# Kernel optimization log

Measured on AMD Instinct MI355X. Metric: run time of the kernel, lower is better.

Reference implementation:

```python
import jax, jax.numpy as jnp
import numpy as np

GRID_SIZE, SPLINE_ORDER = 5, 3
NUM_BASES = GRID_SIZE + SPLINE_ORDER  # 8
GRID = jnp.asarray(np.arange(-SPLINE_ORDER, GRID_SIZE + SPLINE_ORDER + 1, dtype=np.float32) * (2.0 / GRID_SIZE) - 1.0)  # (12,)


def _b_splines(x):
    # x: (M, F) -> (M, F, NUM_BASES), Cox-de Boor recursion on shared uniform grid
    g = GRID
    xe = x[..., None]
    b = ((xe >= g[:-1]) & (xe < g[1:])).astype(x.dtype)
    for k in range(1, SPLINE_ORDER + 1):
        b = ((xe - g[:-(k + 1)]) / (g[k:-1] - g[:-(k + 1)]) * b[..., :-1]
             + (g[k + 1:] - xe) / (g[k + 1:] - g[1:-k]) * b[..., 1:])
    return b


def _kan_linear(x, base_w, spline_w):
    # x: (M, Fin); base_w: (Fout, Fin); spline_w: (Fout, Fin, NUM_BASES)
    base = jax.nn.silu(x) @ base_w.T
    spl = _b_splines(x).reshape(x.shape[0], -1) @ spline_w.reshape(spline_w.shape[0], -1).T
    return base + spl


def _ln(x, g, b, eps=1e-5):
    mu = jnp.mean(x, -1, keepdims=True)
    var = jnp.var(x, -1, keepdims=True)
    return (x - mu) * jax.lax.rsqrt(var + eps) * g + b


def _dwconv(img, w, b):
    C = img.shape[1]
    out = jax.lax.conv_general_dilated(img, w, (1, 1), 'SAME',
        dimension_numbers=('NCHW', 'OIHW', 'NCHW'), feature_group_count=C)
    return out + b[None, :, None, None]


def _dw_bn_relu(x, H, W, w, b, gamma, beta, eps=1e-5):
    # BN in eval mode with running_mean=0, running_var=1
    B, N, C = x.shape
    img = x.transpose(0, 2, 1).reshape(B, C, H, W)
    out = _dwconv(img, w, b)
    out = out * (gamma * (1.0 / np.sqrt(1.0 + eps)))[None, :, None, None] + beta[None, :, None, None]
    out = jax.nn.relu(out)
    return out.reshape(B, C, H * W).transpose(0, 2, 1)


def _cross_selective_scan(img, x_proj_w, dt_w, dt_b, A_logs, Ds, g, b):
    # img: (B, Di, H, W). 4-direction diagonal/antidiagonal selective scan (VMamba-style).
    B, Di, H, W = img.shape
    L = H * W
    K = x_proj_w.shape[0]
    R = dt_w.shape[2]
    Nst = A_logs.shape[1]
    i = jnp.arange(H)[:, None]
    j = jnp.arange(W)[None, :]
    diag = (i + j) % W
    adiag = (j - i) % W
    diag_inv = (jnp.arange(W)[None, :] - i) % W
    adiag_inv = (jnp.arange(W)[None, :] + i) % W

    def gather(x, idx):
        gth = jnp.take_along_axis(x, idx[None, None], axis=3)  # (B,Di,H,W)
        return gth.transpose(0, 1, 3, 2).reshape(B, Di, L)

    def scatter(flat, idx_inv):
        v = flat.reshape(B, Di, W, H).transpose(0, 1, 3, 2)
        return jnp.take_along_axis(v, idx_inv[None, None], axis=3)

    gd, gad = gather(img, diag), gather(img, adiag)
    xs = jnp.stack([gd, gad, jnp.flip(gd, -1), jnp.flip(gad, -1)], axis=1)  # (B,K,Di,L)
    x_dbl = jnp.einsum('bkdl,kcd->bkcl', xs, x_proj_w)
    dts, Bs, Cs = jnp.split(x_dbl, [R, R + Nst], axis=2)  # (B,K,R,L),(B,K,N,L),(B,K,N,L)
    dts = jnp.einsum('bkrl,kdr->bkdl', dts, dt_w)
    delta = jax.nn.softplus(dts + dt_b[None, :, :, None])  # (B,K,Di,L)
    A = -jnp.exp(A_logs).reshape(K, Di, Nst)

    def step(hst, inp):
        u_t, d_t, B_t, C_t = inp  # (B,K,Di),(B,K,Di),(B,K,N),(B,K,N)
        dA = jnp.exp(d_t[..., None] * A)
        hst = dA * hst + (d_t * u_t)[..., None] * B_t[:, :, None, :]
        return hst, jnp.einsum('bkdn,bkn->bkd', hst, C_t)

    h0 = jnp.zeros((B, K, Di, Nst), img.dtype)
    _, ys = jax.lax.scan(step, h0,
        (xs.transpose(3, 0, 1, 2), delta.transpose(3, 0, 1, 2),
         Bs.transpose(3, 0, 1, 2), Cs.transpose(3, 0, 1, 2)))  # ys: (L,B,K,Di)
    ys = ys.transpose(1, 2, 3, 0) + Ds.reshape(K, Di)[None, :, :, None] * xs  # (B,K,Di,L)
    yd = ys[:, 0] + jnp.flip(ys[:, 2], -1)
    ya = ys[:, 1] + jnp.flip(ys[:, 3], -1)
    y = scatter(yd, diag_inv) + scatter(ya, adiag_inv)  # (B,Di,H,W)
    y = y.reshape(B, Di, L).transpose(0, 2, 1)
    return _ln(y, g, b)  # (B,L,Di)


def setup_inputs():
    key = jax.random.key(0)
    ks = iter(jax.random.split(key, 48))
    B, H, W, C = 4, 64, 64, 96
    Di, K, Nst = 2 * C, 4, 16
    R = int(np.ceil(C / 16))
    L = H * W

    def rn(shape, s=0.05):
        return jax.random.normal(next(ks), shape, jnp.float32) * s

    return dict(
        x=jax.random.normal(next(ks), (B, L, C), jnp.float32),
        H=H, W=W,
        norm1_g=jnp.ones((C,), jnp.float32), norm1_b=jnp.zeros((C,), jnp.float32),
        in_proj_w=rn((2 * Di, C)),
        conv_w=rn((Di, 1, 3, 3), 0.2), conv_b=jnp.zeros((Di,), jnp.float32),
        x_proj_w=rn((K, R + 2 * Nst, Di)),
        dt_w=rn((K, Di, R), 0.1), dt_b=rn((K, Di), 0.1),
        A_logs=jax.random.uniform(next(ks), (K * Di, Nst), jnp.float32),
        Ds=jnp.ones((K * Di,), jnp.float32),
        out_norm_g=jnp.ones((Di,), jnp.float32), out_norm_b=jnp.zeros((Di,), jnp.float32),
        out_proj_w=rn((C, Di)),
        norm2_g=jnp.ones((C,), jnp.float32), norm2_b=jnp.zeros((C,), jnp.float32),
        fc1_base_w=rn((C, C)), fc1_spline_w=rn((C, C, NUM_BASES), 0.02),
        fc2_base_w=rn((C, C)), fc2_spline_w=rn((C, C, NUM_BASES), 0.02),
        fc3_base_w=rn((C, C)), fc3_spline_w=rn((C, C, NUM_BASES), 0.02),
        dw1_w=rn((C, 1, 3, 3), 0.2), dw1_b=jnp.zeros((C,), jnp.float32),
        dw1_g=jnp.ones((C,), jnp.float32), dw1_beta=jnp.zeros((C,), jnp.float32),
        dw2_w=rn((C, 1, 3, 3), 0.2), dw2_b=jnp.zeros((C,), jnp.float32),
        dw2_g=jnp.ones((C,), jnp.float32), dw2_beta=jnp.zeros((C,), jnp.float32),
        dw3_w=rn((C, 1, 3, 3), 0.2), dw3_b=jnp.zeros((C,), jnp.float32),
        dw3_g=jnp.ones((C,), jnp.float32), dw3_beta=jnp.zeros((C,), jnp.float32),
    )


def reference(x, H, W, norm1_g, norm1_b, in_proj_w, conv_w, conv_b, x_proj_w,
              dt_w, dt_b, A_logs, Ds, out_norm_g, out_norm_b, out_proj_w,
              norm2_g, norm2_b, fc1_base_w, fc1_spline_w, fc2_base_w, fc2_spline_w,
              fc3_base_w, fc3_spline_w, dw1_w, dw1_b, dw1_g, dw1_beta,
              dw2_w, dw2_b, dw2_g, dw2_beta, dw3_w, dw3_b, dw3_g, dw3_beta):
    B, L, C = x.shape
    # --- SS2D branch ---
    h = _ln(x, norm1_g, norm1_b)
    xz = h @ in_proj_w.T  # (B,L,2*Di)
    Di = xz.shape[-1] // 2
    xin, z = xz[..., :Di], xz[..., Di:]
    img = xin.transpose(0, 2, 1).reshape(B, Di, H, W)
    img = jax.nn.silu(_dwconv(img, conv_w, conv_b))
    y = _cross_selective_scan(img, x_proj_w, dt_w, dt_b, A_logs, Ds, out_norm_g, out_norm_b)
    y = y * jax.nn.silu(z)
    x = x + y @ out_proj_w.T
    # --- KAN branch ---
    h = _ln(x, norm2_g, norm2_b)
    M = B * L
    t = _kan_linear(h.reshape(M, C), fc1_base_w, fc1_spline_w).reshape(B, L, -1)
    t = _dw_bn_relu(t, H, W, dw1_w, dw1_b, dw1_g, dw1_beta)
    t = _kan_linear(t.reshape(M, -1), fc2_base_w, fc2_spline_w).reshape(B, L, -1)
    t = _dw_bn_relu(t, H, W, dw2_w, dw2_b, dw2_g, dw2_beta)
    t = _kan_linear(t.reshape(M, -1), fc3_base_w, fc3_spline_w).reshape(B, L, -1)
    t = _dw_bn_relu(t, H, W, dw3_w, dw3_b, dw3_g, dw3_beta)
    return x + t
```

## Files before the change

kernel.cpp:

```cpp
#include <hip/hip_runtime.h>
#include <math.h>

constexpr int B_  = 4;
constexpr int H_  = 64;
constexpr int W_  = 64;
constexpr int C_  = 96;
constexpr int L_  = H_ * W_;
constexpr int DI  = 192;
constexpr int K_  = 4;
constexpr int NST = 16;
constexpr int R_  = 6;
constexpr int M_  = B_ * L_;

constexpr int NCH = 128;
constexpr int CL  = 32;
constexpr int DG  = 12;

constexpr int KANK = 864;
constexpr int KLAY = 96 * KANK;

typedef __attribute__((ext_vector_type(8))) short short8;
typedef __attribute__((ext_vector_type(4))) float floatx4;
typedef __attribute__((ext_vector_type(4))) unsigned short ushort4v;

__device__ __forceinline__ float wave_sum64(float v) {
#pragma unroll
  for (int off = 1; off < 64; off <<= 1) v += __shfl_xor(v, off, 64);
  return v;
}

__device__ __forceinline__ float exp2_hw(float x) {
  return __builtin_amdgcn_exp2f(x);
}

__device__ __forceinline__ int pos_kl(int k, int l) {
  int ll = (k >= 2) ? (L_ - 1 - l) : l;
  int i = ll & 63;
  int j = ll >> 6;
  int col = ((k & 1) == 0) ? ((i + j) & 63) : ((j - i) & 63);
  return (i << 6) + col;
}

__device__ __forceinline__ int pos_pair(int pr, int ll) {
  int i = ll & 63, j = ll >> 6;
  int col = (pr == 0) ? ((i + j) & 63) : ((j - i) & 63);
  return (i << 6) + col;
}

__device__ __forceinline__ float silu_f(float x) {
  return x / (1.f + __expf(-x));
}

__device__ __forceinline__ float softplus_fast(float s) {
  return fmaxf(s, 0.f) + __logf(1.f + __expf(-fabsf(s)));
}

__device__ __forceinline__ unsigned short f2bf(float f) {
  unsigned u = __float_as_uint(f);
  unsigned r = (u + 0x7FFFu + ((u >> 16) & 1u)) >> 16;
  return (unsigned short)r;
}

__device__ __forceinline__ float bf2f(unsigned short h) {
  return __uint_as_float(((unsigned)h) << 16);
}

__device__ __forceinline__ void spline8(float x, float* bb ) {
#pragma unroll
  for (int i2 = 0; i2 < 11; i2++) {
    float g0 = 0.4f * i2 - 2.2f;
    float g1 = 0.4f * i2 - 1.8f;
    bb[i2] = (x >= g0 && x < g1) ? 1.f : 0.f;
  }
#pragma unroll
  for (int k2 = 1; k2 <= 3; k2++) {
    float invd = 1.f / (0.4f * k2);
#pragma unroll
    for (int i2 = 0; i2 + k2 < 11; i2++) {
      float gi   = 0.4f * i2 - 2.2f;
      float gik1 = 0.4f * (i2 + k2 + 1) - 2.2f;
      bb[i2] = (x - gi) * invd * bb[i2] + (gik1 - x) * invd * bb[i2 + 1];
    }
  }
}

__global__ __launch_bounds__(256) void ln96_kernel(const float* __restrict__ in,
    const float* __restrict__ g, const float* __restrict__ b,
    float* __restrict__ out) {
  int wave = blockIdx.x * 4 + (threadIdx.x >> 6);
  int lane = threadIdx.x & 63;
  const float* rp = in + (size_t)wave * C_;
  float v0 = rp[lane];
  float v1 = (lane < C_ - 64) ? rp[lane + 64] : 0.f;
  float s  = wave_sum64(v0 + v1);
  float s2 = wave_sum64(v0 * v0 + v1 * v1);
  float mean = s * (1.f / C_);
  float var  = s2 * (1.f / C_) - mean * mean;
  float inv  = rsqrtf(var + 1e-5f);
  float* op = out + (size_t)wave * C_;
  op[lane] = (v0 - mean) * inv * g[lane] + b[lane];
  if (lane < C_ - 64) op[lane + 64] = (v1 - mean) * inv * g[lane + 64] + b[lane + 64];
}

__global__ __launch_bounds__(256) void prep_inproj_kernel(const float* __restrict__ w,
    unsigned short* __restrict__ wio) {
  int idx = blockIdx.x * 256 + threadIdx.x;
  if (idx >= 384 * 96) return;
  float v = w[idx];
  unsigned short hh = f2bf(v);
  wio[idx] = hh;
  wio[36864 + idx] = f2bf(v - bf2f(hh));
}

__global__ __launch_bounds__(256) void gemm_in_mfma_kernel(const float* __restrict__ h,
    const unsigned short* __restrict__ wio, float* __restrict__ xin,
    float* __restrict__ z) {
  __shared__ __align__(16) unsigned short Wh[96][104];
  __shared__ __align__(16) unsigned short Wl[96][104];
  int row0 = blockIdx.x * 64;
  int tid = threadIdx.x;
  int wv = tid >> 6, lane = tid & 63, mrow = lane & 15, quad = lane >> 4;

  short8 ah[3], al[3];
  const float* hr = h + (size_t)(row0 + wv * 16 + mrow) * C_;
#pragma unroll
  for (int ks = 0; ks < 3; ks++) {
    float4 va = *(const float4*)&hr[ks * 32 + quad * 8];
    float4 vb = *(const float4*)&hr[ks * 32 + quad * 8 + 4];
    float f[8] = {va.x, va.y, va.z, va.w, vb.x, vb.y, vb.z, vb.w};
    short8 hh, ll;
#pragma unroll
    for (int q = 0; q < 8; q++) {
      unsigned short hv = f2bf(f[q]);
      hh[q] = (short)hv;
      ll[q] = (short)f2bf(f[q] - bf2f(hv));
    }
    ah[ks] = hh; al[ks] = ll;
  }
  for (int nc = 0; nc < 4; nc++) {
    if (nc) __syncthreads();
    for (int t = tid; t < 96 * 12; t += 256) {
      int j = t / 12, u = t % 12;
      *(short8*)&Wh[j][u * 8] = *(const short8*)&wio[(size_t)(nc * 96 + j) * 96 + u * 8];
      *(short8*)&Wl[j][u * 8] = *(const short8*)&wio[(size_t)(384 + nc * 96 + j) * 96 + u * 8];
    }
    __syncthreads();
    floatx4 acc[6];
#pragma unroll
    for (int q = 0; q < 6; q++) acc[q] = (floatx4)(0.f);
#pragma unroll
    for (int ks = 0; ks < 3; ks++) {
#pragma unroll
      for (int nt = 0; nt < 6; nt++) {
        short8 bh = *(const short8*)&Wh[nt * 16 + mrow][ks * 32 + quad * 8];
        short8 bl = *(const short8*)&Wl[nt * 16 + mrow][ks * 32 + quad * 8];
        acc[nt] = __builtin_amdgcn_mfma_f32_16x16x32_bf16(ah[ks], bh, acc[nt], 0, 0, 0);
        acc[nt] = __builtin_amdgcn_mfma_f32_16x16x32_bf16(al[ks], bh, acc[nt], 0, 0, 0);
        acc[nt] = __builtin_amdgcn_mfma_f32_16x16x32_bf16(ah[ks], bl, acc[nt], 0, 0, 0);
      }
    }
#pragma unroll
    for (int nt = 0; nt < 6; nt++) {
      int j = nc * 96 + nt * 16 + mrow;
#pragma unroll
      for (int rg = 0; rg < 4; rg++) {
        int row = row0 + wv * 16 + quad * 4 + rg;
        float v = acc[nt][rg];
        if (j < DI) xin[(size_t)row * DI + j] = v;
        else        z[(size_t)row * DI + (j - DI)] = v;
      }
    }
  }
}

__global__ __launch_bounds__(192) void conv_silu_kernel(const float* __restrict__ xin,
    const float* __restrict__ cw, const float* __restrict__ cb, float* __restrict__ imgT) {
  int p = blockIdx.x;
  int b = p >> 12;
  int ij = p & 4095;
  int i = ij >> 6, j = ij & 63;
  int c = threadIdx.x;
  float acc = cb[c];
#pragma unroll
  for (int di = -1; di <= 1; di++) {
    int ii = i + di;
    if (ii < 0 || ii >= H_) continue;
#pragma unroll
    for (int dj = -1; dj <= 1; dj++) {
      int jj = j + dj;
      if (jj < 0 || jj >= W_) continue;
      acc += xin[((size_t)b * L_ + ii * W_ + jj) * DI + c] * cw[c * 9 + (di + 1) * 3 + (dj + 1)];
    }
  }
  imgT[(size_t)p * DI + c] = silu_f(acc);
}

__global__ __launch_bounds__(256) void xdbl_mfma_kernel(const float* __restrict__ imgT,
    const float* __restrict__ xpw, float* __restrict__ dts_g,
    float* __restrict__ BsT, float* __restrict__ CsT) {
  __shared__ __align__(16) unsigned short Ah[64][104];
  __shared__ __align__(16) unsigned short Al[64][104];
  __shared__ __align__(16) unsigned short Wh[48][104];
  __shared__ __align__(16) unsigned short Wl[48][104];
  __shared__ int pos_s[64];

  int blk = blockIdx.x;
  int lt = blk & 63;
  int bk = blk >> 6;
  int k = bk % K_, b = bk / K_;
  int l0 = lt * 64;
  int tid = threadIdx.x;
  int wid = tid >> 6;
  int lane = tid & 63;
  int mrow = lane & 15, quad = lane >> 4;

  if (tid < 64) pos_s[tid] = pos_kl(k, l0 + tid);
  __syncthreads();

  floatx4 acc[3];
#pragma unroll
  for (int q = 0; q < 3; q++) acc[q] = (floatx4)(0.f);

  const float* img_b = imgT + (size_t)b * L_ * DI;

  for (int kc = 0; kc < 2; kc++) {
    if (kc) __syncthreads();
    for (int t = tid; t < 64 * 24; t += 256) {
      int li = t / 24, c4 = (t % 24) * 4;
      const float4 v = *(const float4*)&img_b[(size_t)pos_s[li] * DI + kc * 96 + c4];
      ushort4v h4, l4;
      float fv[4] = {v.x, v.y, v.z, v.w};
#pragma unroll
      for (int q = 0; q < 4; q++) {
        unsigned short hh = f2bf(fv[q]);
        h4[q] = hh;
        l4[q] = f2bf(fv[q] - bf2f(hh));
      }
      *(ushort4v*)&Ah[li][c4] = h4;
      *(ushort4v*)&Al[li][c4] = l4;
    }
    for (int t = tid; t < 48 * 24; t += 256) {
      int j = t / 24, c4 = (t % 24) * 4;
      ushort4v h4 = (ushort4v)0, l4 = (ushort4v)0;
      if (j < 38) {
        int c = (j < 32) ? (j + 6) : (j - 32);
        const float4 v = *(const float4*)&xpw[((size_t)(k * 38 + c)) * DI + kc * 96 + c4];
        float fv[4] = {v.x, v.y, v.z, v.w};
#pragma unroll
        for (int q = 0; q < 4; q++) {
          unsigned short hh = f2bf(fv[q]);
          h4[q] = hh;
          l4[q] = f2bf(fv[q] - bf2f(hh));
        }
      }
      *(ushort4v*)&Wh[j][c4] = h4;
      *(ushort4v*)&Wl[j][c4] = l4;
    }
    __syncthreads();
#pragma unroll
    for (int ks = 0; ks < 3; ks++) {
      short8 ah = *(const short8*)&Ah[wid * 16 + mrow][ks * 32 + quad * 8];
      short8 al = *(const short8*)&Al[wid * 16 + mrow][ks * 32 + quad * 8];
#pragma unroll
      for (int nt = 0; nt < 3; nt++) {
        short8 bh = *(const short8*)&Wh[nt * 16 + mrow][ks * 32 + quad * 8];
        short8 bl = *(const short8*)&Wl[nt * 16 + mrow][ks * 32 + quad * 8];
        acc[nt] = __builtin_amdgcn_mfma_f32_16x16x32_bf16(ah, bh, acc[nt], 0, 0, 0);
        acc[nt] = __builtin_amdgcn_mfma_f32_16x16x32_bf16(al, bh, acc[nt], 0, 0, 0);
        acc[nt] = __builtin_amdgcn_mfma_f32_16x16x32_bf16(ah, bl, acc[nt], 0, 0, 0);
      }
    }
  }
  size_t bkL = (size_t)(b * K_ + k) * L_ + l0;
#pragma unroll
  for (int rg = 0; rg < 4; rg++) {
    int grow = wid * 16 + quad * 4 + rg;
    size_t base = (bkL + grow) * NST;
    BsT[base + mrow] = acc[0][rg];
    CsT[base + mrow] = acc[1][rg];
    if (mrow < R_) dts_g[(bkL + grow) * 8 + mrow] = acc[2][rg];
  }
}

__global__ __launch_bounds__(192) void scan1_kernel(const float* __restrict__ imgT,
    const float* __restrict__ dts_g, const float* __restrict__ BsT,
    const float* __restrict__ A_logs, const float* __restrict__ dtw,
    const float* __restrict__ dtb, float* __restrict__ hend,
    float* __restrict__ aprod) {
  __shared__ float bs_s[CL][NST];
  __shared__ float dt_s[CL][8];
  int blk = blockIdx.x;
  int c = blk % NCH;
  int tmp = blk / NCH;
  int k = tmp % K_, b = tmp / K_;
  int l0 = c * CL;
  int d = threadIdx.x;
  const float* img_b = imgT + (size_t)b * L_ * DI;
  {
    const float* Bs_bk = BsT + ((size_t)(b * K_ + k) * L_ + l0) * NST;
    for (int t = d; t < CL * NST; t += 192) bs_s[t >> 4][t & 15] = Bs_bk[t];
    const float* Dt = dts_g + ((size_t)(b * K_ + k) * L_ + l0) * 8;
    for (int t = d; t < CL * 8; t += 192) dt_s[t >> 3][t & 7] = Dt[t];
  }
  float A2[NST];
  {
    const float* ap = A_logs + (size_t)(k * DI + d) * NST;
#pragma unroll
    for (int n = 0; n < NST; n++) A2[n] = -__expf(ap[n]) * 1.44269504f;
  }
  float w6[6], bias;
  {
    const float* wp = dtw + ((size_t)k * DI + d) * R_;
#pragma unroll
    for (int r = 0; r < 6; r++) w6[r] = wp[r];
    bias = dtb[k * DI + d];
  }
  __syncthreads();
  float h[NST];
#pragma unroll
  for (int n = 0; n < NST; n++) h[n] = 0.f;
  float sum_dlt = 0.f;
  float u = img_b[(size_t)pos_kl(k, l0) * DI + d];
  for (int l = 0; l < CL; l++) {
    float uc = u;
    if (l + 1 < CL) u = img_b[(size_t)pos_kl(k, l0 + l + 1) * DI + d];
    const float* dv = dt_s[l];
    float s = bias + w6[0] * dv[0] + w6[1] * dv[1] + w6[2] * dv[2]
                   + w6[3] * dv[3] + w6[4] * dv[4] + w6[5] * dv[5];
    float dc = softplus_fast(s);
    sum_dlt += dc;
    float du = dc * uc;
#pragma unroll
    for (int n = 0; n < NST; n++) {
      float dA = exp2_hw(dc * A2[n]);
      h[n] = dA * h[n] + du * bs_s[l][n];
    }
  }
  size_t base = ((size_t)(b * K_ + k) * NCH + c) * (DI * NST) + d;
#pragma unroll
  for (int n = 0; n < NST; n++) {
    hend[base + (size_t)n * DI]  = h[n];
    aprod[base + (size_t)n * DI] = exp2_hw(A2[n] * sum_dlt);
  }
}

__global__ __launch_bounds__(256) void scan_carry_kernel(float* __restrict__ hend,
    const float* __restrict__ aprod) {
  constexpr int PF = 8;
  int blk = blockIdx.x;
  int part = blk % DG;
  int bk = blk / DG;
  const size_t DNS = (size_t)DI * NST;
  size_t base = (size_t)bk * NCH * DNS + (size_t)part * 256 + threadIdx.x;
  float hb[PF], ab[PF];
#pragma unroll
  for (int q = 0; q < PF; q++) {
    hb[q] = hend[base + (size_t)q * DNS];
    ab[q] = aprod[base + (size_t)q * DNS];
  }
  float carry = 0.f;
  for (int c0 = 0; c0 < NCH; c0 += PF) {
    float hn[PF], an[PF];
    if (c0 + PF < NCH) {
#pragma unroll
      for (int q = 0; q < PF; q++) {
        hn[q] = hend[base + (size_t)(c0 + PF + q) * DNS];
        an[q] = aprod[base + (size_t)(c0 + PF + q) * DNS];
      }
    } else {
#pragma unroll
      for (int q = 0; q < PF; q++) { hn[q] = 0.f; an[q] = 0.f; }
    }
#pragma unroll
    for (int q = 0; q < PF; q++) {
      hend[base + (size_t)(c0 + q) * DNS] = carry;
      carry = ab[q] * carry + hb[q];
    }
#pragma unroll
    for (int q = 0; q < PF; q++) { hb[q] = hn[q]; ab[q] = an[q]; }
  }
}

__global__ __launch_bounds__(192) void scan2_pair_kernel(const float* __restrict__ imgT,
    const float* __restrict__ dts_g, const float* __restrict__ BsT,
    const float* __restrict__ CsT, const float* __restrict__ A_logs,
    const float* __restrict__ dtw, const float* __restrict__ dtb,
    const float* __restrict__ Ds, const float* __restrict__ carry_in,
    float* __restrict__ y02, float* __restrict__ y13) {
  __shared__ float bsf[CL][NST], csf[CL][NST], bsr[CL][NST], csr[CL][NST];
  __shared__ float dtf[CL][8], dtr[CL][8];
  __shared__ float y_lds[CL][DI];
  int blk = blockIdx.x;
  int c  = blk % NCH;
  int pr = (blk / NCH) & 1;
  int b  = blk / (2 * NCH);
  int kf = pr, kr = pr + 2;
  int p0 = c * CL;
  int d = threadIdx.x;
  const float* img_b = imgT + (size_t)b * L_ * DI;
  {
    const float* Bf = BsT + ((size_t)(b * K_ + kf) * L_ + p0) * NST;
    const float* Cf = CsT + ((size_t)(b * K_ + kf) * L_ + p0) * NST;
    for (int t = d; t < CL * NST; t += 192) {
      bsf[t >> 4][t & 15] = Bf[t];
      csf[t >> 4][t & 15] = Cf[t];
    }
    const float* Br = BsT + (size_t)(b * K_ + kr) * L_ * NST;
    const float* Cr = CsT + (size_t)(b * K_ + kr) * L_ * NST;
    for (int t = d; t < CL * NST; t += 192) {
      int q = t >> 4, n = t & 15;
      size_t sr = (size_t)(L_ - 1 - p0 - q) * NST + n;
      bsr[q][n] = Br[sr];
      csr[q][n] = Cr[sr];
    }
    const float* Df = dts_g + ((size_t)(b * K_ + kf) * L_ + p0) * 8;
    for (int t = d; t < CL * 8; t += 192) dtf[t >> 3][t & 7] = Df[t];
    const float* Dr = dts_g + (size_t)(b * K_ + kr) * L_ * 8;
    for (int t = d; t < CL * 8; t += 192) {
      int q = t >> 3, r = t & 7;
      dtr[q][r] = Dr[(size_t)(L_ - 1 - p0 - q) * 8 + r];
    }
  }
  __syncthreads();
  float A2[NST], h[NST], w6[6], bias;
  {
    const float* ap = A_logs + (size_t)(kf * DI + d) * NST;
#pragma unroll
    for (int n = 0; n < NST; n++) A2[n] = -__expf(ap[n]) * 1.44269504f;
    size_t cb = ((size_t)(b * K_ + kf) * NCH + c) * (DI * NST) + d;
#pragma unroll
    for (int n = 0; n < NST; n++) h[n] = carry_in[cb + (size_t)n * DI];
    const float* wp = dtw + ((size_t)kf * DI + d) * R_;
#pragma unroll
    for (int r = 0; r < 6; r++) w6[r] = wp[r];
    bias = dtb[kf * DI + d];
  }
  float u = img_b[(size_t)pos_pair(pr, p0) * DI + d];
  for (int q = 0; q < CL; q++) {
    float uc = u;
    if (q + 1 < CL) u = img_b[(size_t)pos_pair(pr, p0 + q + 1) * DI + d];
    const float* dv = dtf[q];
    float s = bias + w6[0] * dv[0] + w6[1] * dv[1] + w6[2] * dv[2]
                   + w6[3] * dv[3] + w6[4] * dv[4] + w6[5] * dv[5];
    float dc = softplus_fast(s);
    float du = dc * uc;
    float yq = 0.f;
#pragma unroll
    for (int n = 0; n < NST; n++) {
      float dA = exp2_hw(dc * A2[n]);
      h[n] = dA * h[n] + du * bsf[q][n];
      yq += h[n] * csf[q][n];
    }
    y_lds[q][d] = yq;
  }
  {
    const float* ap = A_logs + (size_t)(kr * DI + d) * NST;
#pragma unroll
    for (int n = 0; n < NST; n++) A2[n] = -__expf(ap[n]) * 1.44269504f;
    size_t cb = ((size_t)(b * K_ + kr) * NCH + (NCH - 1 - c)) * (DI * NST) + d;
#pragma unroll
    for (int n = 0; n < NST; n++) h[n] = carry_in[cb + (size_t)n * DI];
    const float* wp = dtw + ((size_t)kr * DI + d) * R_;
#pragma unroll
    for (int r = 0; r < 6; r++) w6[r] = wp[r];
    bias = dtb[kr * DI + d];
  }
  float dsum = 0.f;
  if (pr == 0) dsum = Ds[d] + Ds[DI + d] + Ds[2 * DI + d] + Ds[3 * DI + d];
  float* yout = (pr == 0) ? y02 : y13;
  u = img_b[(size_t)pos_pair(pr, p0 + CL - 1) * DI + d];
  for (int q = CL - 1; q >= 0; q--) {
    float uc = u;
    if (q > 0) u = img_b[(size_t)pos_pair(pr, p0 + q - 1) * DI + d];
    const float* dv = dtr[q];
    float s = bias + w6[0] * dv[0] + w6[1] * dv[1] + w6[2] * dv[2]
                   + w6[3] * dv[3] + w6[4] * dv[4] + w6[5] * dv[5];
    float dc = softplus_fast(s);
    float du = dc * uc;
    float yq = y_lds[q][d];
#pragma unroll
    for (int n = 0; n < NST; n++) {
      float dA = exp2_hw(dc * A2[n]);
      h[n] = dA * h[n] + du * bsr[q][n];
      yq += h[n] * csr[q][n];
    }
    if (pr == 0) yq += dsum * uc;
    yout[((size_t)b * L_ + pos_pair(pr, p0 + q)) * DI + d] = yq;
  }
}

__global__ __launch_bounds__(256) void ln_mulz_kernel(const float* __restrict__ y02,
    const float* __restrict__ y13, const float* __restrict__ g,
    const float* __restrict__ bb, float* __restrict__ z) {
  int wave = blockIdx.x * 4 + (threadIdx.x >> 6);
  int lane = threadIdx.x & 63;
  const float* rp = y02 + (size_t)wave * DI;
  const float* rq = y13 + (size_t)wave * DI;
  float v0 = rp[lane]       + rq[lane];
  float v1 = rp[lane + 64]  + rq[lane + 64];
  float v2 = rp[lane + 128] + rq[lane + 128];
  float s  = wave_sum64(v0 + v1 + v2);
  float s2 = wave_sum64(v0 * v0 + v1 * v1 + v2 * v2);
  float mean = s * (1.f / DI);
  float var  = s2 * (1.f / DI) - mean * mean;
  float inv  = rsqrtf(var + 1e-5f);
  float* zp = z + (size_t)wave * DI;
  float vv[3] = {v0, v1, v2};
#pragma unroll
  for (int q = 0; q < 3; q++) {
    int c = lane + 64 * q;
    float zv = zp[c];
    zp[c] = ((vv[q] - mean) * inv * g[c] + bb[c]) * silu_f(zv);
  }
}

__global__ __launch_bounds__(128) void outproj_kernel(const float* __restrict__ yz,
    const float* __restrict__ opw, const float* __restrict__ x, float* __restrict__ x_res) {
  __shared__ float ys[8][DI];
  int row0 = blockIdx.x * 8;
  for (int t = threadIdx.x; t < 8 * DI; t += 128)
    ys[t / DI][t % DI] = yz[(size_t)(row0 + t / DI) * DI + (t % DI)];
  __syncthreads();
  int j = threadIdx.x;
  if (j < C_) {
    float acc[8];
#pragma unroll
    for (int r = 0; r < 8; r++) acc[r] = 0.f;
    const float* wr = opw + (size_t)j * DI;
    for (int d = 0; d < DI; d++) {
      float wv = wr[d];
#pragma unroll
      for (int r = 0; r < 8; r++) acc[r] += wv * ys[r][d];
    }
#pragma unroll
    for (int r = 0; r < 8; r++) {
      size_t row = row0 + r;
      x_res[row * C_ + j] = x[row * C_ + j] + acc[r];
    }
  }
}

__global__ __launch_bounds__(256) void prepw_kernel(const float* __restrict__ bw1,
    const float* __restrict__ sw1, const float* __restrict__ bw2,
    const float* __restrict__ sw2, const float* __restrict__ bw3,
    const float* __restrict__ sw3, unsigned short* __restrict__ wcat) {
  int idx = blockIdx.x * 256 + threadIdx.x;
  if (idx >= 3 * KLAY) return;
  int layer = idx / KLAY, rem = idx % KLAY;
  int j = rem / KANK, k = rem % KANK;
  const float* bw = (layer == 0) ? bw1 : (layer == 1) ? bw2 : bw3;
  const float* sw = (layer == 0) ? sw1 : (layer == 1) ? sw2 : sw3;
  float v = (k < C_) ? bw[j * C_ + k] : sw[j * 768 + (k - C_)];
  wcat[idx] = f2bf(v);
}

__global__ __launch_bounds__(256) void kan_mfma_kernel(const float* __restrict__ in,
    const unsigned short* __restrict__ wl, float* __restrict__ out) {
  __shared__ __align__(16) float x_s[32][100];
  __shared__ __align__(16) unsigned short A_s[32][104];
  __shared__ __align__(16) unsigned short W_s[96][104];
  int row0 = blockIdx.x * 32;
  int tid = threadIdx.x;
  for (int t = tid; t < 32 * 24; t += 256) {
    int r = t / 24, c4 = (t % 24) * 4;
    *(float4*)&x_s[r][c4] = *(const float4*)&in[(size_t)(row0 + r) * C_ + c4];
  }
  floatx4 acc[3];
#pragma unroll
  for (int q = 0; q < 3; q++) acc[q] = (floatx4)(0.f);
  int wv = tid >> 6;
  int rh = wv >> 1, ch = wv & 1;
  int lane = tid & 63;
  int mrow = lane & 15, quad = lane >> 4;
  __syncthreads();
  for (int ci = 0; ci < 9; ci++) {
    if (ci) __syncthreads();
    for (int t = tid; t < 96 * 12; t += 256) {
      int j = t / 12, u = t % 12;
      *(short8*)&W_s[j][u * 8] =
          *(const short8*)&wl[(size_t)j * KANK + ci * 96 + u * 8];
    }
    if (ci == 0) {
      for (int t = tid; t < 32 * 48; t += 256) {
        int r = t / 48, k2 = (t % 48) * 2;
        unsigned v = (unsigned)f2bf(silu_f(x_s[r][k2])) |
                     ((unsigned)f2bf(silu_f(x_s[r][k2 + 1])) << 16);
        *(unsigned*)&A_s[r][k2] = v;
      }
    } else {
      int c0 = (ci - 1) * 12;
      for (int t = tid; t < 32 * 12; t += 256) {
        int r = t & 31, cl = t >> 5;
        float x = x_s[r][c0 + cl];
        float bb[11];
        spline8(x, bb);
        short8 av;
#pragma unroll
        for (int q = 0; q < 8; q++) av[q] = (short)f2bf(bb[q]);
        *(short8*)&A_s[r][cl * 8] = av;
      }
    }
    __syncthreads();
#pragma unroll
    for (int ks = 0; ks < 3; ks++) {
      short8 a = *(const short8*)&A_s[rh * 16 + mrow][ks * 32 + quad * 8];
#pragma unroll
      for (int ct = 0; ct < 3; ct++) {
        short8 b = *(const short8*)&W_s[ch * 48 + ct * 16 + mrow][ks * 32 + quad * 8];
        acc[ct] = __builtin_amdgcn_mfma_f32_16x16x32_bf16(a, b, acc[ct], 0, 0, 0);
      }
    }
  }
#pragma unroll
  for (int ct = 0; ct < 3; ct++)
#pragma unroll
    for (int rg = 0; rg < 4; rg++) {
      int row = row0 + rh * 16 + quad * 4 + rg;
      out[(size_t)row * C_ + ch * 48 + ct * 16 + mrow] = acc[ct][rg];
    }
}

__global__ __launch_bounds__(128) void dwbn_kernel(const float* __restrict__ t,
    const float* __restrict__ w, const float* __restrict__ bias,
    const float* __restrict__ gamma, const float* __restrict__ beta,
    const float* __restrict__ addres, float* __restrict__ out) {
  int p = blockIdx.x;
  int b = p >> 12;
  int ij = p & 4095;
  int i = ij >> 6, j = ij & 63;
  int c = threadIdx.x;
  if (c >= C_) return;
  float acc = bias[c];
#pragma unroll
  for (int di = -1; di <= 1; di++) {
    int ii = i + di;
    if (ii < 0 || ii >= H_) continue;
#pragma unroll
    for (int dj = -1; dj <= 1; dj++) {
      int jj = j + dj;
      if (jj < 0 || jj >= W_) continue;
      acc += t[((size_t)b * L_ + ii * W_ + jj) * C_ + c] * w[c * 9 + (di + 1) * 3 + (dj + 1)];
    }
  }
  float v = acc * (gamma[c] * rsqrtf(1.f + 1e-5f)) + beta[c];
  v = fmaxf(v, 0.f);
  if (addres != nullptr) v += addres[(size_t)p * C_ + c];
  out[(size_t)p * C_ + c] = v;
}

extern "C" void kernel_launch(void* const* d_in, const int* in_sizes, int n_in,
                              void* d_out, int out_size, void* d_ws, size_t ws_size,
                              hipStream_t stream) {
  const float* x         = (const float*)d_in[0];
  const float* norm1_g   = (const float*)d_in[3];
  const float* norm1_b   = (const float*)d_in[4];
  const float* in_proj_w = (const float*)d_in[5];
  const float* conv_w    = (const float*)d_in[6];
  const float* conv_b    = (const float*)d_in[7];
  const float* x_proj_w  = (const float*)d_in[8];
  const float* dt_w      = (const float*)d_in[9];
  const float* dt_b      = (const float*)d_in[10];
  const float* A_logs    = (const float*)d_in[11];
  const float* Ds        = (const float*)d_in[12];
  const float* out_ng    = (const float*)d_in[13];
  const float* out_nb    = (const float*)d_in[14];
  const float* out_proj_w= (const float*)d_in[15];
  const float* norm2_g   = (const float*)d_in[16];
  const float* norm2_b   = (const float*)d_in[17];
  const float* fc1_bw    = (const float*)d_in[18];
  const float* fc1_sw    = (const float*)d_in[19];
  const float* fc2_bw    = (const float*)d_in[20];
  const float* fc2_sw    = (const float*)d_in[21];
  const float* fc3_bw    = (const float*)d_in[22];
  const float* fc3_sw    = (const float*)d_in[23];
  const float* dw1_w     = (const float*)d_in[24];
  const float* dw1_b     = (const float*)d_in[25];
  const float* dw1_g     = (const float*)d_in[26];
  const float* dw1_be    = (const float*)d_in[27];
  const float* dw2_w     = (const float*)d_in[28];
  const float* dw2_b     = (const float*)d_in[29];
  const float* dw2_g     = (const float*)d_in[30];
  const float* dw2_be    = (const float*)d_in[31];
  const float* dw3_w     = (const float*)d_in[32];
  const float* dw3_b     = (const float*)d_in[33];
  const float* dw3_g     = (const float*)d_in[34];
  const float* dw3_be    = (const float*)d_in[35];

  float* ws = (float*)d_ws;
  float* h_buf   = ws;
  float* xin_buf = h_buf + (size_t)M_ * C_;
  float* z_buf   = xin_buf + (size_t)M_ * DI;
  float* imgT    = z_buf + (size_t)M_ * DI;
  float* BsT     = imgT + (size_t)M_ * DI;
  float* CsT     = BsT + (size_t)B_ * K_ * L_ * NST;
  float* y_pre   = CsT + (size_t)B_ * K_ * L_ * NST;
  float* x_res   = y_pre + (size_t)M_ * DI;
  float* t_a     = x_res + (size_t)M_ * C_;
  float* t_b     = t_a + (size_t)M_ * C_;
  float* hend    = t_b + (size_t)M_ * C_;
  float* aprod   = hend + (size_t)B_ * K_ * NCH * DI * NST;
  float* dts_g   = t_a;
  unsigned short* wio  = (unsigned short*)t_b;
  float* y13     = xin_buf;
  unsigned short* wcat = (unsigned short*)BsT;

  ln96_kernel<<<M_ / 4, 256, 0, stream>>>(x, norm1_g, norm1_b, h_buf);
  prep_inproj_kernel<<<144, 256, 0, stream>>>(in_proj_w, wio);
  gemm_in_mfma_kernel<<<M_ / 64, 256, 0, stream>>>(h_buf, wio, xin_buf, z_buf);
  conv_silu_kernel<<<M_, 192, 0, stream>>>(xin_buf, conv_w, conv_b, imgT);
  xdbl_mfma_kernel<<<B_ * K_ * (L_ / 64), 256, 0, stream>>>(imgT, x_proj_w, dts_g,
                                                            BsT, CsT);
  scan1_kernel<<<B_ * K_ * NCH, 192, 0, stream>>>(imgT, dts_g, BsT, A_logs,
                                                  dt_w, dt_b, hend, aprod);
  scan_carry_kernel<<<B_ * K_ * DG, 256, 0, stream>>>(hend, aprod);
  scan2_pair_kernel<<<B_ * 2 * NCH, 192, 0, stream>>>(imgT, dts_g, BsT, CsT, A_logs,
                                                      dt_w, dt_b, Ds, hend,
                                                      y_pre, y13);
  prepw_kernel<<<(3 * KLAY + 255) / 256, 256, 0, stream>>>(fc1_bw, fc1_sw, fc2_bw,
                                                           fc2_sw, fc3_bw, fc3_sw, wcat);
  ln_mulz_kernel<<<M_ / 4, 256, 0, stream>>>(y_pre, y13, out_ng, out_nb, z_buf);
  outproj_kernel<<<M_ / 8, 128, 0, stream>>>(z_buf, out_proj_w, x, x_res);
  ln96_kernel<<<M_ / 4, 256, 0, stream>>>(x_res, norm2_g, norm2_b, h_buf);
  kan_mfma_kernel<<<M_ / 32, 256, 0, stream>>>(h_buf, wcat, t_a);
  dwbn_kernel<<<M_, 128, 0, stream>>>(t_a, dw1_w, dw1_b, dw1_g, dw1_be, nullptr, t_b);
  kan_mfma_kernel<<<M_ / 32, 256, 0, stream>>>(t_b, wcat + KLAY, t_a);
  dwbn_kernel<<<M_, 128, 0, stream>>>(t_a, dw2_w, dw2_b, dw2_g, dw2_be, nullptr, t_b);
  kan_mfma_kernel<<<M_ / 32, 256, 0, stream>>>(t_b, wcat + 2 * KLAY, t_a);
  dwbn_kernel<<<M_, 128, 0, stream>>>(t_a, dw3_w, dw3_b, dw3_g, dw3_be, x_res, (float*)d_out);
}
```

Measured before the change: 506.8 us.

## Preload scan inputs into registers, precompute A2, keep y in registers, pack dwbn

Adds a small kernel that computes -exp(A_logs)*log2e once, and the scan kernels load that table with vector loads. scan1 and scan2 now fetch all 32 u values of a chunk into registers before the barrier and compute the softplus deltas in a separate pass. The reverse scan accumulates into a y register array in place of a shared-memory buffer, and B/C rows are read as float4 vectors. dwbn now handles two pixels per 192-thread block so no threads sit idle. The cost is higher register pressure from the 32-element arrays, which may reduce occupancy. The A2 table also needs extra workspace beyond aprod.

```diff
diff --git a/kernel.cpp b/kernel.cpp
--- a/kernel.cpp
+++ b/kernel.cpp
@@ -112,6 +112,12 @@
   wio[36864 + idx] = f2bf(v - bf2f(hh));
 }
 
+__global__ __launch_bounds__(256) void prep_a2_kernel(const float* __restrict__ A_logs,
+    float* __restrict__ a2g) {
+  int idx = blockIdx.x * 256 + threadIdx.x;
+  if (idx < K_ * DI * NST) a2g[idx] = -__expf(A_logs[idx]) * 1.44269504f;
+}
+
 __global__ __launch_bounds__(256) void gemm_in_mfma_kernel(const float* __restrict__ h,
     const unsigned short* __restrict__ wio, float* __restrict__ xin,
     float* __restrict__ z) {
@@ -284,7 +290,7 @@
 
 __global__ __launch_bounds__(192) void scan1_kernel(const float* __restrict__ imgT,
     const float* __restrict__ dts_g, const float* __restrict__ BsT,
-    const float* __restrict__ A_logs, const float* __restrict__ dtw,
+    const float* __restrict__ a2g, const float* __restrict__ dtw,
     const float* __restrict__ dtb, float* __restrict__ hend,
     float* __restrict__ aprod) {
   __shared__ float bs_s[CL][NST];
@@ -304,9 +310,12 @@
   }
   float A2[NST];
   {
-    const float* ap = A_logs + (size_t)(k * DI + d) * NST;
-#pragma unroll
-    for (int n = 0; n < NST; n++) A2[n] = -__expf(ap[n]) * 1.44269504f;
+    const floatx4* ap = (const floatx4*)(a2g + (size_t)(k * DI + d) * NST);
+#pragma unroll
+    for (int i = 0; i < 4; i++) {
+      floatx4 v = ap[i];
+      A2[4 * i] = v[0]; A2[4 * i + 1] = v[1]; A2[4 * i + 2] = v[2]; A2[4 * i + 3] = v[3];
+    }
   }
   float w6[6], bias;
   {
@@ -315,25 +324,36 @@
     for (int r = 0; r < 6; r++) w6[r] = wp[r];
     bias = dtb[k * DI + d];
   }
+  float u[CL];
+#pragma unroll
+  for (int q = 0; q < CL; q++)
+    u[q] = img_b[(size_t)pos_kl(k, l0 + q) * DI + d];
   __syncthreads();
+  float dc[CL];
+  float sum_dlt = 0.f;
+#pragma unroll
+  for (int q = 0; q < CL; q++) {
+    const floatx4* dp = (const floatx4*)&dt_s[q][0];
+    floatx4 d0 = dp[0], d1 = dp[1];
+    float s = bias + w6[0] * d0[0] + w6[1] * d0[1] + w6[2] * d0[2]
+                   + w6[3] * d0[3] + w6[4] * d1[0] + w6[5] * d1[1];
+    dc[q] = softplus_fast(s);
+    sum_dlt += dc[q];
+  }
   float h[NST];
 #pragma unroll
   for (int n = 0; n < NST; n++) h[n] = 0.f;
-  float sum_dlt = 0.f;
-  float u = img_b[(size_t)pos_kl(k, l0) * DI + d];
-  for (int l = 0; l < CL; l++) {
-    float uc = u;
-    if (l + 1 < CL) u = img_b[(size_t)pos_kl(k, l0 + l + 1) * DI + d];
-    const float* dv = dt_s[l];
-    float s = bias + w6[0] * dv[0] + w6[1] * dv[1] + w6[2] * dv[2]
-                   + w6[3] * dv[3] + w6[4] * dv[4] + w6[5] * dv[5];
-    float dc = softplus_fast(s);
-    sum_dlt += dc;
-    float du = dc * uc;
+#pragma unroll
+  for (int q = 0; q < CL; q++) {
+    float du = dc[q] * u[q];
+    floatx4 bsv[4];
+    const floatx4* bp = (const floatx4*)&bs_s[q][0];
+#pragma unroll
+    for (int i = 0; i < 4; i++) bsv[i] = bp[i];
 #pragma unroll
     for (int n = 0; n < NST; n++) {
-      float dA = exp2_hw(dc * A2[n]);
-      h[n] = dA * h[n] + du * bs_s[l][n];
+      float dA = exp2_hw(dc[q] * A2[n]);
+      h[n] = dA * h[n] + du * bsv[n >> 2][n & 3];
     }
   }
   size_t base = ((size_t)(b * K_ + k) * NCH + c) * (DI * NST) + d;
@@ -383,13 +403,12 @@
 
 __global__ __launch_bounds__(192) void scan2_pair_kernel(const float* __restrict__ imgT,
     const float* __restrict__ dts_g, const float* __restrict__ BsT,
-    const float* __restrict__ CsT, const float* __restrict__ A_logs,
+    const float* __restrict__ CsT, const float* __restrict__ a2g,
     const float* __restrict__ dtw, const float* __restrict__ dtb,
     const float* __restrict__ Ds, const float* __restrict__ carry_in,
     float* __restrict__ y02, float* __restrict__ y13) {
   __shared__ float bsf[CL][NST], csf[CL][NST], bsr[CL][NST], csr[CL][NST];
   __shared__ float dtf[CL][8], dtr[CL][8];
-  __shared__ float y_lds[CL][DI];
   int blk = blockIdx.x;
   int c  = blk % NCH;
   int pr = (blk / NCH) & 1;
@@ -421,12 +440,23 @@
       dtr[q][r] = Dr[(size_t)(L_ - 1 - p0 - q) * 8 + r];
     }
   }
+  float u[CL], y[CL];
+#pragma unroll
+  for (int q = 0; q < CL; q++)
+    u[q] = img_b[(size_t)pos_pair(pr, p0 + q) * DI + d];
+  float dsum = 0.f;
+  if (pr == 0) dsum = Ds[d] + Ds[DI + d] + Ds[2 * DI + d] + Ds[3 * DI + d];
+#pragma unroll
+  for (int q = 0; q < CL; q++) y[q] = dsum * u[q];
   __syncthreads();
-  float A2[NST], h[NST], w6[6], bias;
+  float A2[NST], h[NST], w6[6], bias, dc[CL];
   {
-    const float* ap = A_logs + (size_t)(kf * DI + d) * NST;
-#pragma unroll
-    for (int n = 0; n < NST; n++) A2[n] = -__expf(ap[n]) * 1.44269504f;
+    const floatx4* ap = (const floatx4*)(a2g + (size_t)(kf * DI + d) * NST);
+#pragma unroll
+    for (int i = 0; i < 4; i++) {
+      floatx4 v = ap[i];
+      A2[4 * i] = v[0]; A2[4 * i + 1] = v[1]; A2[4 * i + 2] = v[2]; A2[4 * i + 3] = v[3];
+    }
     size_t cb = ((size_t)(b * K_ + kf) * NCH + c) * (DI * NST) + d;
 #pragma unroll
     for (int n = 0; n < NST; n++) h[n] = carry_in[cb + (size_t)n * DI];
@@ -435,28 +465,38 @@
     for (int r = 0; r < 6; r++) w6[r] = wp[r];
     bias = dtb[kf * DI + d];
   }
-  float u = img_b[(size_t)pos_pair(pr, p0) * DI + d];
+#pragma unroll
   for (int q = 0; q < CL; q++) {
-    float uc = u;
-    if (q + 1 < CL) u = img_b[(size_t)pos_pair(pr, p0 + q + 1) * DI + d];
-    const float* dv = dtf[q];
-    float s = bias + w6[0] * dv[0] + w6[1] * dv[1] + w6[2] * dv[2]
-                   + w6[3] * dv[3] + w6[4] * dv[4] + w6[5] * dv[5];
-    float dc = softplus_fast(s);
-    float du = dc * uc;
-    float yq = 0.f;
+    const floatx4* dp = (const floatx4*)&dtf[q][0];
+    floatx4 d0 = dp[0], d1 = dp[1];
+    float s = bias + w6[0] * d0[0] + w6[1] * d0[1] + w6[2] * d0[2]
+                   + w6[3] * d0[3] + w6[4] * d1[0] + w6[5] * d1[1];
+    dc[q] = softplus_fast(s);
+  }
+#pragma unroll
+  for (int q = 0; q < CL; q++) {
+    float du = dc[q] * u[q];
+    floatx4 bsv[4], csv[4];
+    const floatx4* bp = (const floatx4*)&bsf[q][0];
+    const floatx4* cp = (const floatx4*)&csf[q][0];
+#pragma unroll
+    for (int i = 0; i < 4; i++) { bsv[i] = bp[i]; csv[i] = cp[i]; }
+    float yq = y[q];
 #pragma unroll
     for (int n = 0; n < NST; n++) {
-      float dA = exp2_hw(dc * A2[n]);
-      h[n] = dA * h[n] + du * bsf[q][n];
-      yq += h[n] * csf[q][n];
-    }
-    y_lds[q][d] = yq;
+      float dA = exp2_hw(dc[q] * A2[n]);
+      h[n] = dA * h[n] + du * bsv[n >> 2][n & 3];
+      yq += h[n] * csv[n >> 2][n & 3];
+    }
+    y[q] = yq;
   }
   {
-    const float* ap = A_logs + (size_t)(kr * DI + d) * NST;
-#pragma unroll
-    for (int n = 0; n < NST; n++) A2[n] = -__expf(ap[n]) * 1.44269504f;
+    const floatx4* ap = (const floatx4*)(a2g + (size_t)(kr * DI + d) * NST);
+#pragma unroll
+    for (int i = 0; i < 4; i++) {
+      floatx4 v = ap[i];
+      A2[4 * i] = v[0]; A2[4 * i + 1] = v[1]; A2[4 * i + 2] = v[2]; A2[4 * i + 3] = v[3];
+    }
     size_t cb = ((size_t)(b * K_ + kr) * NCH + (NCH - 1 - c)) * (DI * NST) + d;
 #pragma unroll
     for (int n = 0; n < NST; n++) h[n] = carry_in[cb + (size_t)n * DI];
@@ -465,28 +505,36 @@
     for (int r = 0; r < 6; r++) w6[r] = wp[r];
     bias = dtb[kr * DI + d];
   }
-  float dsum = 0.f;
-  if (pr == 0) dsum = Ds[d] + Ds[DI + d] + Ds[2 * DI + d] + Ds[3 * DI + d];
+#pragma unroll
+  for (int q = 0; q < CL; q++) {
+    const floatx4* dp = (const floatx4*)&dtr[q][0];
+    floatx4 d0 = dp[0], d1 = dp[1];
+    float s = bias + w6[0] * d0[0] + w6[1] * d0[1] + w6[2] * d0[2]
+                   + w6[3] * d0[3] + w6[4] * d1[0] + w6[5] * d1[1];
+    dc[q] = softplus_fast(s);
+  }
+#pragma unroll
+  for (int qq = 0; qq < CL; qq++) {
+    int q = CL - 1 - qq;
+    float du = dc[q] * u[q];
+    floatx4 bsv[4], csv[4];
+    const floatx4* bp = (const floatx4*)&bsr[q][0];
+    const floatx4* cp = (const floatx4*)&csr[q][0];
+#pragma unroll
+    for (int i = 0; i < 4; i++) { bsv[i] = bp[i]; csv[i] = cp[i]; }
+    float yq = y[q];
+#pragma unroll
+    for (int n = 0; n < NST; n++) {
+      float dA = exp2_hw(dc[q] * A2[n]);
+      h[n] = dA * h[n] + du * bsv[n >> 2][n & 3];
+      yq += h[n] * csv[n >> 2][n & 3];
+    }
+    y[q] = yq;
+  }
   float* yout = (pr == 0) ? y02 : y13;
-  u = img_b[(size_t)pos_pair(pr, p0 + CL - 1) * DI + d];
-  for (int q = CL - 1; q >= 0; q--) {
-    float uc = u;
-    if (q > 0) u = img_b[(size_t)pos_pair(pr, p0 + q - 1) * DI + d];
-    const float* dv = dtr[q];
-    float s = bias + w6[0] * dv[0] + w6[1] * dv[1] + w6[2] * dv[2]
-                   + w6[3] * dv[3] + w6[4] * dv[4] + w6[5] * dv[5];
-    float dc = softplus_fast(s);
-    float du = dc * uc;
-    float yq = y_lds[q][d];
-#pragma unroll
-    for (int n = 0; n < NST; n++) {
-      float dA = exp2_hw(dc * A2[n]);
-      h[n] = dA * h[n] + du * bsr[q][n];
-      yq += h[n] * csr[q][n];
-    }
-    if (pr == 0) yq += dsum * uc;
-    yout[((size_t)b * L_ + pos_pair(pr, p0 + q)) * DI + d] = yq;
-  }
+#pragma unroll
+  for (int q = 0; q < CL; q++)
+    yout[((size_t)b * L_ + pos_pair(pr, p0 + q)) * DI + d] = y[q];
 }
 
 __global__ __launch_bounds__(256) void ln_mulz_kernel(const float* __restrict__ y02,
@@ -620,16 +668,17 @@
     }
 }
 
-__global__ __launch_bounds__(128) void dwbn_kernel(const float* __restrict__ t,
+__global__ __launch_bounds__(192) void dwbn_kernel(const float* __restrict__ t,
     const float* __restrict__ w, const float* __restrict__ bias,
     const float* __restrict__ gamma, const float* __restrict__ beta,
     const float* __restrict__ addres, float* __restrict__ out) {
-  int p = blockIdx.x;
+  int tid = threadIdx.x;
+  int half = (tid >= 96) ? 1 : 0;
+  int c = tid - half * 96;
+  int p = blockIdx.x * 2 + half;
   int b = p >> 12;
   int ij = p & 4095;
   int i = ij >> 6, j = ij & 63;
-  int c = threadIdx.x;
-  if (c >= C_) return;
   float acc = bias[c];
 #pragma unroll
   for (int di = -1; di <= 1; di++) {
@@ -699,6 +748,7 @@
   float* t_b     = t_a + (size_t)M_ * C_;
   float* hend    = t_b + (size_t)M_ * C_;
   float* aprod   = hend + (size_t)B_ * K_ * NCH * DI * NST;
+  float* a2_buf  = aprod + (size_t)B_ * K_ * NCH * DI * NST;
   float* dts_g   = t_a;
   unsigned short* wio  = (unsigned short*)t_b;
   float* y13     = xin_buf;
@@ -706,14 +756,15 @@
 
   ln96_kernel<<<M_ / 4, 256, 0, stream>>>(x, norm1_g, norm1_b, h_buf);
   prep_inproj_kernel<<<144, 256, 0, stream>>>(in_proj_w, wio);
+  prep_a2_kernel<<<48, 256, 0, stream>>>(A_logs, a2_buf);
   gemm_in_mfma_kernel<<<M_ / 64, 256, 0, stream>>>(h_buf, wio, xin_buf, z_buf);
   conv_silu_kernel<<<M_, 192, 0, stream>>>(xin_buf, conv_w, conv_b, imgT);
   xdbl_mfma_kernel<<<B_ * K_ * (L_ / 64), 256, 0, stream>>>(imgT, x_proj_w, dts_g,
                                                             BsT, CsT);
-  scan1_kernel<<<B_ * K_ * NCH, 192, 0, stream>>>(imgT, dts_g, BsT, A_logs,
+  scan1_kernel<<<B_ * K_ * NCH, 192, 0, stream>>>(imgT, dts_g, BsT, a2_buf,
                                                   dt_w, dt_b, hend, aprod);
   scan_carry_kernel<<<B_ * K_ * DG, 256, 0, stream>>>(hend, aprod);
-  scan2_pair_kernel<<<B_ * 2 * NCH, 192, 0, stream>>>(imgT, dts_g, BsT, CsT, A_logs,
+  scan2_pair_kernel<<<B_ * 2 * NCH, 192, 0, stream>>>(imgT, dts_g, BsT, CsT, a2_buf,
                                                       dt_w, dt_b, Ds, hend,
                                                       y_pre, y13);
   prepw_kernel<<<(3 * KLAY + 255) / 256, 256, 0, stream>>>(fc1_bw, fc1_sw, fc2_bw,
@@ -722,9 +773,9 @@
   outproj_kernel<<<M_ / 8, 128, 0, stream>>>(z_buf, out_proj_w, x, x_res);
   ln96_kernel<<<M_ / 4, 256, 0, stream>>>(x_res, norm2_g, norm2_b, h_buf);
   kan_mfma_kernel<<<M_ / 32, 256, 0, stream>>>(h_buf, wcat, t_a);
-  dwbn_kernel<<<M_, 128, 0, stream>>>(t_a, dw1_w, dw1_b, dw1_g, dw1_be, nullptr, t_b);
+  dwbn_kernel<<<M_ / 2, 192, 0, stream>>>(t_a, dw1_w, dw1_b, dw1_g, dw1_be, nullptr, t_b);
   kan_mfma_kernel<<<M_ / 32, 256, 0, stream>>>(t_b, wcat + KLAY, t_a);
-  dwbn_kernel<<<M_, 128, 0, stream>>>(t_a, dw2_w, dw2_b, dw2_g, dw2_be, nullptr, t_b);
+  dwbn_kernel<<<M_ / 2, 192, 0, stream>>>(t_a, dw2_w, dw2_b, dw2_g, dw2_be, nullptr, t_b);
   kan_mfma_kernel<<<M_ / 32, 256, 0, stream>>>(t_b, wcat + 2 * KLAY, t_a);
-  dwbn_kernel<<<M_, 128, 0, stream>>>(t_a, dw3_w, dw3_b, dw3_g, dw3_be, x_res, (float*)d_out);
-}
+  dwbn_kernel<<<M_ / 2, 192, 0, stream>>>(t_a, dw3_w, dw3_b, dw3_g, dw3_be, x_res, (float*)d_out);
+}
```

Measured after the change: 489.5 us. 1.04x faster.
